# Performance work log

Measured on AMD Instinct MI355X. Metric: run time of the kernel, lower is better.

## Reference

```python
import jax, jax.numpy as jnp
import numpy as np

K = 64        # num_clusters
S1 = 5        # num_shadow + 1
C = 128       # dim
ALPHA = 1500.0
EPS = 1e-12


def setup_inputs() -> dict:
    key = jax.random.key(0)
    k1, k2 = jax.random.split(key)
    x = jax.random.normal(k1, (8, C, 44, 44), dtype=jnp.float32)
    centroids = jax.random.normal(k2, (K, S1, C), dtype=jnp.float32) * 0.01
    return {"x": x, "centroids": centroids}


def reference(x, centroids):
    N = x.shape[0]
    # conv params derived from centroids, as in _init_params
    w = (2.0 * ALPHA) * centroids.reshape(K * S1, C)            # (K*S1, C)
    b = -ALPHA * jnp.linalg.norm(centroids.reshape(K * S1, C), axis=1)  # (K*S1,)

    xf = x.reshape(N, C, -1)                                    # (N, C, P)
    # 1x1 conv == GEMM over channel dim
    logits = jnp.einsum('mc,ncp->nmp', w, xf) + b[None, :, None]
    logits = logits.reshape(N, K, S1, -1)                       # (N, K, S1, P)

    soft_alpha = jax.nn.softmax(logits[:, :, 0:1, :], axis=1)   # (N, K, 1, P)
    soft_beta = jax.nn.softmax(logits, axis=2)[:, :, 0:1, :]    # (N, K, 1, P)
    soft_assign = soft_alpha * soft_beta                        # (N, K, 1, P)

    # residual = x - rep_centroid; then residual *= (1 + soft_assign); sum over P.
    # sum_p (x[n,c,p] - rep[k,c]) * w[n,k,p]
    #   = einsum(w, x) - rep[k,c] * sum_p w[n,k,p]   (same math, no (N,K,C,P) tensor)
    w_assign = 1.0 + soft_assign[:, :, 0, :]                    # (N, K, P)
    rep = centroids[:, 0, :]                                    # (K, C)
    out = jnp.einsum('nkp,ncp->nkc', w_assign, xf) \
          - rep[None, :, :] * jnp.sum(w_assign, axis=-1)[:, :, None]  # (N, K, C)

    # intra-cluster L2 normalize (dim=2), flatten, global L2 normalize
    out = out / jnp.maximum(jnp.linalg.norm(out, axis=2, keepdims=True), EPS)
    flat = out.reshape(N, -1)
    flat = flat / jnp.maximum(jnp.linalg.norm(flat, axis=1, keepdims=True), EPS)
    return (flat, soft_assign)
```

## Files before the change

kernel.cpp:

```cpp
#include <hip/hip_runtime.h>
#include <math.h>

#define NB 8
#define KC 64
#define S1C 5
#define CC 128
#define PP 1936
#define MM 320
#define PT 64
#define NPT 31
#define NTILE (NB * NPT)
#define ALPHAF 1500.0f
#define EPSF 1e-12f

#define WS_PS   ((size_t)NTILE * KC * CC)
#define WS_MAIN_FLOATS (WS_PS + (size_t)NTILE * KC)
#define WS_FB_ZERO_BYTES ((size_t)(NB * KC * CC + NB * KC) * 4)

typedef __attribute__((ext_vector_type(8))) short short8;
typedef __attribute__((ext_vector_type(4))) float f32x4;

__device__ __forceinline__ unsigned pack_bf16s(float x) {
    unsigned u  = __float_as_uint(x);
    unsigned hi = u & 0xffff0000u;
    float lo    = x - __uint_as_float(hi);
    return hi | (__float_as_uint(lo) >> 16);
}

__device__ __forceinline__ void unpack8(const int4 q0, const int4 q1,
                                        short8& h, short8& l) {
    const int d[8] = {q0.x, q0.y, q0.z, q0.w, q1.x, q1.y, q1.z, q1.w};
#pragma unroll
    for (int j = 0; j < 8; ++j) {
        h[j] = (short)((unsigned)d[j] >> 16);
        l[j] = (short)((unsigned)d[j] & 0xffffu);
    }
}

__device__ __forceinline__ void split8(const float4 a, const float4 b,
                                       short8& h, short8& l) {
    const float f[8] = {a.x, a.y, a.z, a.w, b.x, b.y, b.z, b.w};
#pragma unroll
    for (int j = 0; j < 8; ++j) {
        const unsigned u  = __float_as_uint(f[j]);
        const unsigned hi = u & 0xffff0000u;
        const float lo    = f[j] - __uint_as_float(hi);
        h[j] = (short)(hi >> 16);
        l[j] = (short)(__float_as_uint(lo) >> 16);
    }
}

__global__ __launch_bounds__(1024, 4) void k1_main(
    const float* __restrict__ x, const float* __restrict__ cen,
    float* __restrict__ sa_out, float* __restrict__ outC,
    float* __restrict__ outS, int mode)
{
    __shared__ unsigned xbuf[CC * 68];
    __shared__ unsigned war[KC * 68];
    __shared__ float2   ap[16 * 66];
    __shared__ float    bias_p[512];

    const int tid  = threadIdx.x;
    const int lane = tid & 63;
    const int wid  = tid >> 6;
    const int quad = lane >> 4;
    const int l15  = lane & 15;
    const int bx   = blockIdx.x;
    const int n    = bx / NPT;
    const int pt   = bx - n * NPT;
    const int p0   = pt * PT;

    const float* xn = x + (size_t)n * CC * PP;
    for (int idx = tid; idx < CC * 16; idx += 1024) {
        const int c = idx >> 4;
        const int q = idx & 15;
        const int p = 4 * q;
        float4 v = make_float4(0.f, 0.f, 0.f, 0.f);
        if (p0 + p < PP) v = *(const float4*)(xn + (size_t)c * PP + p0 + p);
        xbuf[(p + 0) * 132 + c] = pack_bf16s(v.x);
        xbuf[(p + 1) * 132 + c] = pack_bf16s(v.y);
        xbuf[(p + 2) * 132 + c] = pack_bf16s(v.z);
        xbuf[(p + 3) * 132 + c] = pack_bf16s(v.w);
    }
    if (tid < 192) bias_p[8 * (tid / 3) + 5 + (tid % 3)] = -3.0e38f;
    if (tid < MM) {
        const float4* row = (const float4*)(cen + (size_t)tid * CC);
        float ss = 0.f;
#pragma unroll
        for (int c4 = 0; c4 < 32; ++c4) {
            const float4 v = row[c4];
            ss += v.x * v.x + v.y * v.y + v.z * v.z + v.w * v.w;
        }
        bias_p[8 * (tid / 5) + (tid % 5)] = -ALPHAF * sqrtf(ss);
    }
    __syncthreads();

    f32x4 dacc[4][2];
#pragma unroll
    for (int a = 0; a < 4; ++a) {
        dacc[a][0] = (f32x4){0.f, 0.f, 0.f, 0.f};
        dacc[a][1] = (f32x4){0.f, 0.f, 0.f, 0.f};
    }
    int mp[2], wrow[2]; bool wvalid[2];
#pragma unroll
    for (int i = 0; i < 2; ++i) {
        mp[i] = (2 * wid + i) * 16 + l15;
        const int s = mp[i] & 7;
        wvalid[i] = (s < 5);
        wrow[i] = 5 * (mp[i] >> 3) + s;
    }

#pragma unroll 1
    for (int ks = 0; ks < 4; ++ks) {
        short8 bh[2], bl[2];
#pragma unroll
        for (int i = 0; i < 2; ++i) {
            float4 wlo = make_float4(0.f, 0.f, 0.f, 0.f);
            float4 whi = make_float4(0.f, 0.f, 0.f, 0.f);
            if (wvalid[i]) {
                const float* wp = cen + (size_t)wrow[i] * CC + ks * 32 + quad * 8;
                wlo = *(const float4*)wp;
                whi = *(const float4*)(wp + 4);
            }
            split8(wlo, whi, bh[i], bl[i]);
        }
#pragma unroll
        for (int a = 0; a < 4; ++a) {
            const int abase = (a * 16 + l15) * 132 + ks * 32 + quad * 8;
            const int4 q0 = *(const int4*)(&xbuf[abase]);
            const int4 q1 = *(const int4*)(&xbuf[abase + 4]);
            short8 ah, al;
            unpack8(q0, q1, ah, al);
#pragma unroll
            for (int i = 0; i < 2; ++i) {
                dacc[a][i] = __builtin_amdgcn_mfma_f32_16x16x32_bf16(ah, bh[i], dacc[a][i], 0, 0, 0);
                dacc[a][i] = __builtin_amdgcn_mfma_f32_16x16x32_bf16(ah, bl[i], dacc[a][i], 0, 0, 0);
                dacc[a][i] = __builtin_amdgcn_mfma_f32_16x16x32_bf16(al, bh[i], dacc[a][i], 0, 0, 0);
            }
        }
    }

    const float bv0 = bias_p[mp[0]];
    const float bv1 = bias_p[mp[1]];
#pragma unroll
    for (int a = 0; a < 4; ++a)
#pragma unroll
        for (int r = 0; r < 4; ++r) {
            dacc[a][0][r] = 2.f * ALPHAF * dacc[a][0][r] + bv0;
            dacc[a][1][r] = 2.f * ALPHAF * dacc[a][1][r] + bv1;
        }

#pragma unroll
    for (int a = 0; a < 4; ++a) {
        f32x4 mx4, se4;
#pragma unroll
        for (int r = 0; r < 4; ++r) {
            float m_ = fmaxf(dacc[a][0][r], dacc[a][1][r]);
            m_ = fmaxf(m_, __shfl_xor(m_, 8));
            float se = __expf(dacc[a][0][r] - m_) + __expf(dacc[a][1][r] - m_);
            se += __shfl_xor(se, 8);
            mx4[r] = m_; se4[r] = se;
        }
        if (l15 == 0) {
#pragma unroll
            for (int r = 0; r < 4; ++r)
                ap[wid * 66 + a * 16 + 4 * quad + r] = make_float2(mx4[r], se4[r]);
        }
    }
    __syncthreads();

    float gmv, arv;
    {
        float gm = -3.0e38f;
#pragma unroll
        for (int w = 0; w < 16; ++w) gm = fmaxf(gm, ap[w * 66 + lane].x);
        float s = 0.f;
#pragma unroll
        for (int w = 0; w < 16; ++w) {
            const float2 v = ap[w * 66 + lane];
            s += v.y * __expf(v.x - gm);
        }
        gmv = gm; arv = 1.0f / s;
    }

    float* san = sa_out + (size_t)n * KC * PP;
    float psum[2] = {0.f, 0.f};
    const bool is_s0 = ((l15 & 7) == 0);
#pragma unroll
    for (int a = 0; a < 4; ++a) {
#pragma unroll
        for (int i = 0; i < 2; ++i) {
            const f32x4 lg = dacc[a][i];
            f32x4 sav; unsigned wpk[4];
#pragma unroll
            for (int r = 0; r < 4; ++r) {
                float m_ = lg[r];
                m_ = fmaxf(m_, __shfl_xor(m_, 1));
                m_ = fmaxf(m_, __shfl_xor(m_, 2));
                m_ = fmaxf(m_, __shfl_xor(m_, 4));
                const float e_ = __expf(lg[r] - m_);
                float d_ = e_;
                d_ += __shfl_xor(d_, 1);
                d_ += __shfl_xor(d_, 2);
                d_ += __shfl_xor(d_, 4);
                const int p = a * 16 + 4 * quad + r;
                const float gm_p = __shfl(gmv, p);
                const float ar_p = __shfl(arv, p);
                const float sa = __expf(lg[r] - gm_p) * ar_p * (e_ / d_);
                const bool pvalid = (p0 + p) < PP;
                const float wa = pvalid ? (1.0f + sa) : 0.0f;
                sav[r] = sa;
                wpk[r] = pack_bf16s(wa);
                psum[i] += wa;
            }
            const int k = 4 * wid + 2 * i + (l15 >> 3);
            if (is_s0) {
                *(int4*)(&war[k * 68 + a * 16 + 4 * quad]) = *(const int4*)wpk;
                const int pg = p0 + a * 16 + 4 * quad;
                if (pg < PP) *(float4*)(&san[(size_t)k * PP + pg]) = *(const float4*)&sav;
            }
        }
    }
#pragma unroll
    for (int i = 0; i < 2; ++i) {
        float s = psum[i];
        s += __shfl_xor(s, 16);
        s += __shfl_xor(s, 32);
        if (is_s0 && quad == 0) {
            const int k = 4 * wid + 2 * i + (l15 >> 3);
            if (mode == 0) outS[(size_t)bx * KC + k] = s;
            else           atomicAdd(&outS[(size_t)n * KC + k], s);
        }
    }
    {
        const int c  = tid >> 3;
        const int po = (tid & 7) * 8;
        float4 v0 = make_float4(0.f, 0.f, 0.f, 0.f), v1 = v0;
        if (p0 + po < PP) {
            const float* src = xn + (size_t)c * PP + p0 + po;
            v0 = *(const float4*)src;
            v1 = *(const float4*)(src + 4);
        }
        unsigned pk[8];
        pk[0] = pack_bf16s(v0.x); pk[1] = pack_bf16s(v0.y);
        pk[2] = pack_bf16s(v0.z); pk[3] = pack_bf16s(v0.w);
        pk[4] = pack_bf16s(v1.x); pk[5] = pack_bf16s(v1.y);
        pk[6] = pack_bf16s(v1.z); pk[7] = pack_bf16s(v1.w);
        *(int4*)(&xbuf[c * 68 + po])     = *(const int4*)&pk[0];
        *(int4*)(&xbuf[c * 68 + po + 4]) = *(const int4*)&pk[4];
    }
    __syncthreads();

    const int kt  = wid & 3;
    const int ct0 = (wid >> 2) * 2;
    f32x4 cacc[2];
    cacc[0] = (f32x4){0.f, 0.f, 0.f, 0.f};
    cacc[1] = (f32x4){0.f, 0.f, 0.f, 0.f};
#pragma unroll
    for (int ks = 0; ks < 64; ks += 32) {
        const int abase = (kt * 16 + l15) * 68 + ks + quad * 8;
        const int4 qa0 = *(const int4*)(&war[abase]);
        const int4 qa1 = *(const int4*)(&war[abase + 4]);
        short8 ah, al;
        unpack8(qa0, qa1, ah, al);
#pragma unroll
        for (int t = 0; t < 2; ++t) {
            const int c = (ct0 + t) * 16 + l15;
            const int bbase = c * 68 + ks + quad * 8;
            const int4 qb0 = *(const int4*)(&xbuf[bbase]);
            const int4 qb1 = *(const int4*)(&xbuf[bbase + 4]);
            short8 bh, bl;
            unpack8(qb0, qb1, bh, bl);
            cacc[t] = __builtin_amdgcn_mfma_f32_16x16x32_bf16(ah, bh, cacc[t], 0, 0, 0);
            cacc[t] = __builtin_amdgcn_mfma_f32_16x16x32_bf16(ah, bl, cacc[t], 0, 0, 0);
            cacc[t] = __builtin_amdgcn_mfma_f32_16x16x32_bf16(al, bh, cacc[t], 0, 0, 0);
        }
    }
    if (mode == 0) {
        float* dst = outC + (size_t)bx * KC * CC;
#pragma unroll
        for (int t = 0; t < 2; ++t) {
            const int c = (ct0 + t) * 16 + l15;
#pragma unroll
            for (int r = 0; r < 4; ++r)
                dst[(kt * 16 + 4 * quad + r) * CC + c] = cacc[t][r];
        }
    } else {
        float* dst = outC + (size_t)n * KC * CC;
#pragma unroll
        for (int t = 0; t < 2; ++t) {
            const int c = (ct0 + t) * 16 + l15;
#pragma unroll
            for (int r = 0; r < 4; ++r)
                atomicAdd(&dst[(kt * 16 + 4 * quad + r) * CC + c], cacc[t][r]);
        }
    }
}

__global__ __launch_bounds__(128) void k2_slab(
    const float* __restrict__ part, const float* __restrict__ ps,
    const float* __restrict__ cen, float* __restrict__ flat)
{
    __shared__ float w2[2];
    const int b = blockIdx.x;
    const int n = b >> 6;
    const int k = b & 63;
    const int c = threadIdx.x;
    const float* pb = part + (size_t)n * NPT * KC * CC + (size_t)k * CC + c;
    float v = 0.f;
#pragma unroll 8
    for (int pt = 0; pt < NPT; ++pt) v += pb[(size_t)pt * KC * CC];
    const float* psb = ps + (size_t)n * NPT * KC + k;
    float sw = 0.f;
#pragma unroll
    for (int pt = 0; pt < NPT; ++pt) sw += psb[(size_t)pt * KC];
    v -= cen[(size_t)k * S1C * CC + c] * sw;

    float ss = v * v;
#pragma unroll
    for (int off = 32; off > 0; off >>= 1) ss += __shfl_down(ss, off);
    if ((c & 63) == 0) w2[c >> 6] = ss;
    __syncthreads();
    const float norm = sqrtf(w2[0] + w2[1]);
    const float scale = 1.0f / (fmaxf(norm, EPSF) * 8.0f);
    flat[(size_t)b * CC + c] = v * scale;
}

__global__ __launch_bounds__(128) void k2_final(
    const float* __restrict__ accC, const float* __restrict__ accS,
    const float* __restrict__ cen, float* __restrict__ flat)
{
    __shared__ float w2[2];
    const int b = blockIdx.x;
    const int k = b & 63;
    const int c = threadIdx.x;
    const float v = accC[(size_t)b * CC + c] -
                    cen[(size_t)k * S1C * CC + c] * accS[b];
    float ss = v * v;
#pragma unroll
    for (int off = 32; off > 0; off >>= 1) ss += __shfl_down(ss, off);
    if ((c & 63) == 0) w2[c >> 6] = ss;
    __syncthreads();
    const float norm = sqrtf(w2[0] + w2[1]);
    const float scale = 1.0f / (fmaxf(norm, EPSF) * 8.0f);
    flat[(size_t)b * CC + c] = v * scale;
}

extern "C" void kernel_launch(void* const* d_in, const int* in_sizes, int n_in,
                              void* d_out, int out_size, void* d_ws, size_t ws_size,
                              hipStream_t stream) {
    const float* x   = (const float*)d_in[0];
    const float* cen = (const float*)d_in[1];
    float* out  = (float*)d_out;
    float* flat = out;
    float* sa   = out + (size_t)NB * KC * CC;
    float* ws   = (float*)d_ws;

    if (ws_size >= WS_MAIN_FLOATS * 4) {
        float* part = ws;
        float* ps   = ws + WS_PS;
        k1_main<<<NTILE, 1024, 0, stream>>>(x, cen, sa, part, ps, 0);
        k2_slab<<<NB * KC, 128, 0, stream>>>(part, ps, cen, flat);
    } else {
        float* accC = ws;
        float* accS = ws + NB * KC * CC;
        hipMemsetAsync(d_ws, 0, WS_FB_ZERO_BYTES, stream);
        k1_main<<<NTILE, 1024, 0, stream>>>(x, cen, sa, accC, accS, 1);
        k2_final<<<NB * KC, 128, 0, stream>>>(accC, accS, cen, flat);
    }
}
```

Measured before the change: 94.41 us.

## Prepack centroids in a separate kernel and halve pixel tile to 32

Adds a small pre-kernel that splits the centroids into bf16 hi/lo pairs in MFMA fragment order and computes the bias once, so each main block no longer recomputes centroid norms or splits weights. The main kernel drops to 512 threads with a 32-pixel tile, which doubles the block count and reworks the warp-to-tile mapping (each warp now covers four M tiles). It also keeps a channel-major x copy in LDS instead of reloading x from global for the second GEMM. In exchange there is an extra kernel launch and twice as many partial slabs for the reduction kernel to sum.

Measured after the change: 106.5 us. +12.8%, slower.

```diff
diff --git a/kernel.cpp b/kernel.cpp
--- a/kernel.cpp
+++ b/kernel.cpp
@@ -6,16 +6,17 @@
 #define S1C 5
 #define CC 128
 #define PP 1936
-#define MM 320
-#define PT 64
-#define NPT 31
+#define PT 32
+#define NPT 61
 #define NTILE (NB * NPT)
 #define ALPHAF 1500.0f
 #define EPSF 1e-12f
 
-#define WS_PS   ((size_t)NTILE * KC * CC)
-#define WS_MAIN_FLOATS (WS_PS + (size_t)NTILE * KC)
-#define WS_FB_ZERO_BYTES ((size_t)(NB * KC * CC + NB * KC) * 4)
+#define WS_CENPK 65536
+#define WS_GBIAS 512
+#define WS_HDR   (WS_CENPK + WS_GBIAS)
+#define WS_PART  ((size_t)NTILE * KC * CC)
+#define WS_MAIN_FLOATS (WS_HDR + WS_PART + (size_t)NTILE * KC)
 
 typedef __attribute__((ext_vector_type(8))) short short8;
 typedef __attribute__((ext_vector_type(4))) float f32x4;
@@ -50,14 +51,51 @@
     }
 }
 
-__global__ __launch_bounds__(1024, 4) void k1_main(
-    const float* __restrict__ x, const float* __restrict__ cen,
+__global__ __launch_bounds__(64) void k0_pack(
+    const float* __restrict__ cen, unsigned* __restrict__ cenPk,
+    float* __restrict__ gbias)
+{
+    const int nt   = blockIdx.x;
+    const int l    = threadIdx.x;
+    const int l15  = l & 15;
+    const int quad = l >> 4;
+    const int mp   = nt * 16 + l15;
+    const int s    = mp & 7;
+    const bool valid = (s < 5);
+    const int wrow = 5 * (mp >> 3) + s;
+    short8* dst8 = (short8*)cenPk;
+    float ss = 0.f;
+#pragma unroll
+    for (int ks = 0; ks < 4; ++ks) {
+        float4 v0 = make_float4(0.f, 0.f, 0.f, 0.f), v1 = v0;
+        if (valid) {
+            const float* wp = cen + (size_t)wrow * CC + ks * 32 + quad * 8;
+            v0 = *(const float4*)wp;
+            v1 = *(const float4*)(wp + 4);
+        }
+        ss += v0.x * v0.x + v0.y * v0.y + v0.z * v0.z + v0.w * v0.w
+            + v1.x * v1.x + v1.y * v1.y + v1.z * v1.z + v1.w * v1.w;
+        short8 h, lo;
+        split8(v0, v1, h, lo);
+        const int base = ((ks * 32 + nt) * 64 + l) * 2;
+        dst8[base]     = h;
+        dst8[base + 1] = lo;
+    }
+    ss += __shfl_xor(ss, 16);
+    ss += __shfl_xor(ss, 32);
+    if (quad == 0) gbias[mp] = valid ? (-ALPHAF * sqrtf(ss)) : -3.0e38f;
+}
+
+__global__ __launch_bounds__(512, 4) void k1_main(
+    const float* __restrict__ x, const unsigned* __restrict__ cenPk,
+    const float* __restrict__ gbias,
     float* __restrict__ sa_out, float* __restrict__ outC,
     float* __restrict__ outS, int mode)
 {
-    __shared__ unsigned xbuf[CC * 68];
-    __shared__ unsigned war[KC * 68];
-    __shared__ float2   ap[16 * 66];
+    __shared__ unsigned xbuf[PT * 132];
+    __shared__ unsigned xc[CC * 36];
+    __shared__ unsigned war[KC * 36];
+    __shared__ float2   ap[8 * 66];
     __shared__ float    bias_p[512];
 
     const int tid  = threadIdx.x;
@@ -71,93 +109,80 @@
     const int p0   = pt * PT;
 
     const float* xn = x + (size_t)n * CC * PP;
-    for (int idx = tid; idx < CC * 16; idx += 1024) {
-        const int c = idx >> 4;
-        const int q = idx & 15;
-        const int p = 4 * q;
-        float4 v = make_float4(0.f, 0.f, 0.f, 0.f);
-        if (p0 + p < PP) v = *(const float4*)(xn + (size_t)c * PP + p0 + p);
-        xbuf[(p + 0) * 132 + c] = pack_bf16s(v.x);
-        xbuf[(p + 1) * 132 + c] = pack_bf16s(v.y);
-        xbuf[(p + 2) * 132 + c] = pack_bf16s(v.z);
-        xbuf[(p + 3) * 132 + c] = pack_bf16s(v.w);
-    }
-    if (tid < 192) bias_p[8 * (tid / 3) + 5 + (tid % 3)] = -3.0e38f;
-    if (tid < MM) {
-        const float4* row = (const float4*)(cen + (size_t)tid * CC);
-        float ss = 0.f;
-#pragma unroll
-        for (int c4 = 0; c4 < 32; ++c4) {
-            const float4 v = row[c4];
-            ss += v.x * v.x + v.y * v.y + v.z * v.z + v.w * v.w;
-        }
-        bias_p[8 * (tid / 5) + (tid % 5)] = -ALPHAF * sqrtf(ss);
-    }
-    __syncthreads();
-
-    f32x4 dacc[4][2];
-#pragma unroll
-    for (int a = 0; a < 4; ++a) {
-        dacc[a][0] = (f32x4){0.f, 0.f, 0.f, 0.f};
-        dacc[a][1] = (f32x4){0.f, 0.f, 0.f, 0.f};
-    }
-    int mp[2], wrow[2]; bool wvalid[2];
-#pragma unroll
-    for (int i = 0; i < 2; ++i) {
-        mp[i] = (2 * wid + i) * 16 + l15;
-        const int s = mp[i] & 7;
-        wvalid[i] = (s < 5);
-        wrow[i] = 5 * (mp[i] >> 3) + s;
-    }
-
+    {
+        const int c  = tid >> 2;
+        const int po = (tid & 3) * 8;
+        float4 v0 = make_float4(0.f, 0.f, 0.f, 0.f), v1 = v0;
+        if (p0 + po < PP) {
+            const float* src = xn + (size_t)c * PP + p0 + po;
+            v0 = *(const float4*)src;
+            v1 = *(const float4*)(src + 4);
+        }
+        unsigned pk[8];
+        pk[0] = pack_bf16s(v0.x); pk[1] = pack_bf16s(v0.y);
+        pk[2] = pack_bf16s(v0.z); pk[3] = pack_bf16s(v0.w);
+        pk[4] = pack_bf16s(v1.x); pk[5] = pack_bf16s(v1.y);
+        pk[6] = pack_bf16s(v1.z); pk[7] = pack_bf16s(v1.w);
+        *(int4*)(&xc[c * 36 + po])     = *(const int4*)&pk[0];
+        *(int4*)(&xc[c * 36 + po + 4]) = *(const int4*)&pk[4];
+#pragma unroll
+        for (int j = 0; j < 8; ++j) xbuf[(po + j) * 132 + c] = pk[j];
+    }
+    bias_p[tid] = gbias[tid];
+    __syncthreads();
+
+    f32x4 dacc[2][4];
+#pragma unroll
+    for (int a = 0; a < 2; ++a)
+#pragma unroll
+        for (int i = 0; i < 4; ++i)
+            dacc[a][i] = (f32x4){0.f, 0.f, 0.f, 0.f};
+
+    const short8* cpk8 = (const short8*)cenPk;
 #pragma unroll 1
     for (int ks = 0; ks < 4; ++ks) {
-        short8 bh[2], bl[2];
-#pragma unroll
-        for (int i = 0; i < 2; ++i) {
-            float4 wlo = make_float4(0.f, 0.f, 0.f, 0.f);
-            float4 whi = make_float4(0.f, 0.f, 0.f, 0.f);
-            if (wvalid[i]) {
-                const float* wp = cen + (size_t)wrow[i] * CC + ks * 32 + quad * 8;
-                wlo = *(const float4*)wp;
-                whi = *(const float4*)(wp + 4);
-            }
-            split8(wlo, whi, bh[i], bl[i]);
-        }
-#pragma unroll
-        for (int a = 0; a < 4; ++a) {
+        short8 ah[2], al[2];
+#pragma unroll
+        for (int a = 0; a < 2; ++a) {
             const int abase = (a * 16 + l15) * 132 + ks * 32 + quad * 8;
             const int4 q0 = *(const int4*)(&xbuf[abase]);
             const int4 q1 = *(const int4*)(&xbuf[abase + 4]);
-            short8 ah, al;
-            unpack8(q0, q1, ah, al);
-#pragma unroll
-            for (int i = 0; i < 2; ++i) {
-                dacc[a][i] = __builtin_amdgcn_mfma_f32_16x16x32_bf16(ah, bh[i], dacc[a][i], 0, 0, 0);
-                dacc[a][i] = __builtin_amdgcn_mfma_f32_16x16x32_bf16(ah, bl[i], dacc[a][i], 0, 0, 0);
-                dacc[a][i] = __builtin_amdgcn_mfma_f32_16x16x32_bf16(al, bh[i], dacc[a][i], 0, 0, 0);
+            unpack8(q0, q1, ah[a], al[a]);
+        }
+#pragma unroll
+        for (int i = 0; i < 4; ++i) {
+            const int boff = ((ks * 32 + 4 * wid + i) * 64 + lane) * 2;
+            const short8 bh = cpk8[boff];
+            const short8 bl = cpk8[boff + 1];
+#pragma unroll
+            for (int a = 0; a < 2; ++a) {
+                dacc[a][i] = __builtin_amdgcn_mfma_f32_16x16x32_bf16(ah[a], bh, dacc[a][i], 0, 0, 0);
+                dacc[a][i] = __builtin_amdgcn_mfma_f32_16x16x32_bf16(ah[a], bl, dacc[a][i], 0, 0, 0);
+                dacc[a][i] = __builtin_amdgcn_mfma_f32_16x16x32_bf16(al[a], bh, dacc[a][i], 0, 0, 0);
             }
         }
     }
 
-    const float bv0 = bias_p[mp[0]];
-    const float bv1 = bias_p[mp[1]];
-#pragma unroll
-    for (int a = 0; a < 4; ++a)
+#pragma unroll
+    for (int i = 0; i < 4; ++i) {
+        const float bv = bias_p[(4 * wid + i) * 16 + l15];
+#pragma unroll
+        for (int a = 0; a < 2; ++a)
+#pragma unroll
+            for (int r = 0; r < 4; ++r)
+                dacc[a][i][r] = 2.f * ALPHAF * dacc[a][i][r] + bv;
+    }
+
+#pragma unroll
+    for (int a = 0; a < 2; ++a) {
+        f32x4 mx4, se4;
 #pragma unroll
         for (int r = 0; r < 4; ++r) {
-            dacc[a][0][r] = 2.f * ALPHAF * dacc[a][0][r] + bv0;
-            dacc[a][1][r] = 2.f * ALPHAF * dacc[a][1][r] + bv1;
-        }
-
-#pragma unroll
-    for (int a = 0; a < 4; ++a) {
-        f32x4 mx4, se4;
-#pragma unroll
-        for (int r = 0; r < 4; ++r) {
-            float m_ = fmaxf(dacc[a][0][r], dacc[a][1][r]);
+            float m_ = fmaxf(fmaxf(dacc[a][0][r], dacc[a][1][r]),
+                             fmaxf(dacc[a][2][r], dacc[a][3][r]));
             m_ = fmaxf(m_, __shfl_xor(m_, 8));
-            float se = __expf(dacc[a][0][r] - m_) + __expf(dacc[a][1][r] - m_);
+            float se = __expf(dacc[a][0][r] - m_) + __expf(dacc[a][1][r] - m_)
+                     + __expf(dacc[a][2][r] - m_) + __expf(dacc[a][3][r] - m_);
             se += __shfl_xor(se, 8);
             mx4[r] = m_; se4[r] = se;
         }
@@ -173,23 +198,23 @@
     {
         float gm = -3.0e38f;
 #pragma unroll
-        for (int w = 0; w < 16; ++w) gm = fmaxf(gm, ap[w * 66 + lane].x);
-        float s = 0.f;
-#pragma unroll
-        for (int w = 0; w < 16; ++w) {
+        for (int w = 0; w < 8; ++w) gm = fmaxf(gm, ap[w * 66 + lane].x);
+        float ssum = 0.f;
+#pragma unroll
+        for (int w = 0; w < 8; ++w) {
             const float2 v = ap[w * 66 + lane];
-            s += v.y * __expf(v.x - gm);
-        }
-        gmv = gm; arv = 1.0f / s;
+            ssum += v.y * __expf(v.x - gm);
+        }
+        gmv = gm; arv = 1.0f / ssum;
     }
 
     float* san = sa_out + (size_t)n * KC * PP;
-    float psum[2] = {0.f, 0.f};
+    float psum[4] = {0.f, 0.f, 0.f, 0.f};
     const bool is_s0 = ((l15 & 7) == 0);
 #pragma unroll
-    for (int a = 0; a < 4; ++a) {
-#pragma unroll
-        for (int i = 0; i < 2; ++i) {
+    for (int a = 0; a < 2; ++a) {
+#pragma unroll
+        for (int i = 0; i < 4; ++i) {
             const f32x4 lg = dacc[a][i];
             f32x4 sav; unsigned wpk[4];
 #pragma unroll
@@ -213,73 +238,55 @@
                 wpk[r] = pack_bf16s(wa);
                 psum[i] += wa;
             }
-            const int k = 4 * wid + 2 * i + (l15 >> 3);
+            const int k = 8 * wid + 2 * i + (l15 >> 3);
             if (is_s0) {
-                *(int4*)(&war[k * 68 + a * 16 + 4 * quad]) = *(const int4*)wpk;
+                *(int4*)(&war[k * 36 + a * 16 + 4 * quad]) = *(const int4*)wpk;
                 const int pg = p0 + a * 16 + 4 * quad;
                 if (pg < PP) *(float4*)(&san[(size_t)k * PP + pg]) = *(const float4*)&sav;
             }
         }
     }
 #pragma unroll
-    for (int i = 0; i < 2; ++i) {
+    for (int i = 0; i < 4; ++i) {
         float s = psum[i];
         s += __shfl_xor(s, 16);
         s += __shfl_xor(s, 32);
         if (is_s0 && quad == 0) {
-            const int k = 4 * wid + 2 * i + (l15 >> 3);
+            const int k = 8 * wid + 2 * i + (l15 >> 3);
             if (mode == 0) outS[(size_t)bx * KC + k] = s;
             else           atomicAdd(&outS[(size_t)n * KC + k], s);
         }
     }
+    __syncthreads();
+
+    const int kt  = wid & 3;
+    const int ct0 = (wid >> 2) * 4;
+    short8 ah2, al2;
     {
-        const int c  = tid >> 3;
-        const int po = (tid & 7) * 8;
-        float4 v0 = make_float4(0.f, 0.f, 0.f, 0.f), v1 = v0;
-        if (p0 + po < PP) {
-            const float* src = xn + (size_t)c * PP + p0 + po;
-            v0 = *(const float4*)src;
-            v1 = *(const float4*)(src + 4);
-        }
-        unsigned pk[8];
-        pk[0] = pack_bf16s(v0.x); pk[1] = pack_bf16s(v0.y);
-        pk[2] = pack_bf16s(v0.z); pk[3] = pack_bf16s(v0.w);
-        pk[4] = pack_bf16s(v1.x); pk[5] = pack_bf16s(v1.y);
-        pk[6] = pack_bf16s(v1.z); pk[7] = pack_bf16s(v1.w);
-        *(int4*)(&xbuf[c * 68 + po])     = *(const int4*)&pk[0];
-        *(int4*)(&xbuf[c * 68 + po + 4]) = *(const int4*)&pk[4];
-    }
-    __syncthreads();
-
-    const int kt  = wid & 3;
-    const int ct0 = (wid >> 2) * 2;
-    f32x4 cacc[2];
-    cacc[0] = (f32x4){0.f, 0.f, 0.f, 0.f};
-    cacc[1] = (f32x4){0.f, 0.f, 0.f, 0.f};
-#pragma unroll
-    for (int ks = 0; ks < 64; ks += 32) {
-        const int abase = (kt * 16 + l15) * 68 + ks + quad * 8;
+        const int abase = (kt * 16 + l15) * 36 + quad * 8;
         const int4 qa0 = *(const int4*)(&war[abase]);
         const int4 qa1 = *(const int4*)(&war[abase + 4]);
-        short8 ah, al;
-        unpack8(qa0, qa1, ah, al);
-#pragma unroll
-        for (int t = 0; t < 2; ++t) {
-            const int c = (ct0 + t) * 16 + l15;
-            const int bbase = c * 68 + ks + quad * 8;
-            const int4 qb0 = *(const int4*)(&xbuf[bbase]);
-            const int4 qb1 = *(const int4*)(&xbuf[bbase + 4]);
-            short8 bh, bl;
-            unpack8(qb0, qb1, bh, bl);
-            cacc[t] = __builtin_amdgcn_mfma_f32_16x16x32_bf16(ah, bh, cacc[t], 0, 0, 0);
-            cacc[t] = __builtin_amdgcn_mfma_f32_16x16x32_bf16(ah, bl, cacc[t], 0, 0, 0);
-            cacc[t] = __builtin_amdgcn_mfma_f32_16x16x32_bf16(al, bh, cacc[t], 0, 0, 0);
-        }
+        unpack8(qa0, qa1, ah2, al2);
+    }
+    f32x4 cacc[4];
+#pragma unroll
+    for (int t = 0; t < 4; ++t) cacc[t] = (f32x4){0.f, 0.f, 0.f, 0.f};
+#pragma unroll
+    for (int t = 0; t < 4; ++t) {
+        const int c = (ct0 + t) * 16 + l15;
+        const int bbase = c * 36 + quad * 8;
+        const int4 qb0 = *(const int4*)(&xc[bbase]);
+        const int4 qb1 = *(const int4*)(&xc[bbase + 4]);
+        short8 bh, bl;
+        unpack8(qb0, qb1, bh, bl);
+        cacc[t] = __builtin_amdgcn_mfma_f32_16x16x32_bf16(ah2, bh, cacc[t], 0, 0, 0);
+        cacc[t] = __builtin_amdgcn_mfma_f32_16x16x32_bf16(ah2, bl, cacc[t], 0, 0, 0);
+        cacc[t] = __builtin_amdgcn_mfma_f32_16x16x32_bf16(al2, bh, cacc[t], 0, 0, 0);
     }
     if (mode == 0) {
         float* dst = outC + (size_t)bx * KC * CC;
 #pragma unroll
-        for (int t = 0; t < 2; ++t) {
+        for (int t = 0; t < 4; ++t) {
             const int c = (ct0 + t) * 16 + l15;
 #pragma unroll
             for (int r = 0; r < 4; ++r)
@@ -288,7 +295,7 @@
     } else {
         float* dst = outC + (size_t)n * KC * CC;
 #pragma unroll
-        for (int t = 0; t < 2; ++t) {
+        for (int t = 0; t < 4; ++t) {
             const int c = (ct0 + t) * 16 + l15;
 #pragma unroll
             for (int r = 0; r < 4; ++r)
@@ -308,11 +315,11 @@
     const int c = threadIdx.x;
     const float* pb = part + (size_t)n * NPT * KC * CC + (size_t)k * CC + c;
     float v = 0.f;
-#pragma unroll 8
+#pragma unroll 4
     for (int pt = 0; pt < NPT; ++pt) v += pb[(size_t)pt * KC * CC];
     const float* psb = ps + (size_t)n * NPT * KC + k;
     float sw = 0.f;
-#pragma unroll
+#pragma unroll 4
     for (int pt = 0; pt < NPT; ++pt) sw += psb[(size_t)pt * KC];
     v -= cen[(size_t)k * S1C * CC + c] * sw;
 
@@ -356,16 +363,21 @@
     float* sa   = out + (size_t)NB * KC * CC;
     float* ws   = (float*)d_ws;
 
+    unsigned* cenPk = (unsigned*)ws;
+    float*    gbias = ws + WS_CENPK;
+
     if (ws_size >= WS_MAIN_FLOATS * 4) {
-        float* part = ws;
-        float* ps   = ws + WS_PS;
-        k1_main<<<NTILE, 1024, 0, stream>>>(x, cen, sa, part, ps, 0);
+        float* part = ws + WS_HDR;
+        float* ps   = part + WS_PART;
+        k0_pack<<<32, 64, 0, stream>>>(cen, cenPk, gbias);
+        k1_main<<<NTILE, 512, 0, stream>>>(x, cenPk, gbias, sa, part, ps, 0);
         k2_slab<<<NB * KC, 128, 0, stream>>>(part, ps, cen, flat);
     } else {
-        float* accC = ws;
-        float* accS = ws + NB * KC * CC;
-        hipMemsetAsync(d_ws, 0, WS_FB_ZERO_BYTES, stream);
-        k1_main<<<NTILE, 1024, 0, stream>>>(x, cen, sa, accC, accS, 1);
+        float* accC = ws + WS_HDR;
+        float* accS = accC + (size_t)NB * KC * CC;
+        hipMemsetAsync(accC, 0, (size_t)(NB * KC * CC + NB * KC) * 4, stream);
+        k0_pack<<<32, 64, 0, stream>>>(cen, cenPk, gbias);
+        k1_main<<<NTILE, 512, 0, stream>>>(x, cenPk, gbias, sa, accC, accS, 1);
         k2_final<<<NB * KC, 128, 0, stream>>>(accC, accS, cen, flat);
     }
 }
```
